# Optimization experiments

Hardware: AMD Instinct MI355X
Metric: run time of the kernel (lower is better)

## Reference

```python
import jax, jax.numpy as jnp
import numpy as np

K0, K1 = 5, 5          # patch_size
PAD = K0 // 2          # 2


def _patches(x, k0, k1):
    """x: [B, Hp, Wp, C] -> [B, Ho, Wo, C, k0*k1] sliding patches (row-major within patch)."""
    B, Hp, Wp, C = x.shape
    Ho, Wo = Hp - k0 + 1, Wp - k1 + 1
    ps = [x[:, i:i + Ho, j:j + Wo, :] for i in range(k0) for j in range(k1)]
    return jnp.stack(ps, axis=-1)


def _normalize(p):
    # per-patch zero-mean / unit (population) std over the k0*k1 patch elements
    m = jnp.mean(p, axis=-1, keepdims=True)
    s = jnp.sqrt(jnp.mean((p - m) ** 2, axis=-1, keepdims=True))
    return (p - m) / s


def setup_inputs() -> dict:
    key = jax.random.key(0)
    k1, k2 = jax.random.split(key)
    B, H, W, C = 8, 32, 32, 64
    input_1 = jax.random.normal(k1, (B, H, W, C), dtype=jnp.float32)
    input_2 = jax.random.normal(k2, (B, H, W, C), dtype=jnp.float32)
    return {"input_1": input_1, "input_2": input_2}


def reference(input_1, input_2):
    B, H, W, C = input_1.shape
    # pad input_1 by PAD on all spatial sides; input_2 by 2*PAD on rows, PAD on cols
    x1 = jnp.pad(input_1, ((0, 0), (PAD, PAD), (PAD, PAD), (0, 0)))
    x2 = jnp.pad(input_2, ((0, 0), (2 * PAD, 2 * PAD), (PAD, PAD), (0, 0)))

    P1 = _normalize(_patches(x1, K0, K1))      # [B, H, W, C, 25]
    P2 = _patches(x2, K0, K1)                  # [B, H+4, W, C, 25] (start rows 0..H+3)

    # Faithful row ordering of the original loops over input_2 patches:
    #   [0..PAD-1] ++ [PAD..H+PAD-1] ++ [H..H+PAD-1]  (rows H,H+1 duplicated; H+2,H+3 unused)
    rows_idx = np.concatenate([np.arange(PAD), np.arange(PAD, H + PAD), np.arange(H, H + PAD)])
    P2 = _normalize(P2[:, rows_idx])           # [B, H+2*PAD, W, C, 25]

    # sliding window of K0 list-rows for each output row r -> rows r..r+K0-1
    P2win = jnp.stack([P2[:, e:e + H] for e in range(K0)], axis=2)  # [B, H, K0, W, C, 25]

    # out[b,r,w,k,e,f] = sum_p P1[b,r,w,k,p] * P2win[b,r,e,f,k,p]
    out = jnp.einsum('brwkp,brefkp->brwkef', P1, P2win)  # [B, H, W, C, K0, W]
    out = out.reshape(B, H, W, C * K0 * W)
    return out  # activation is None (linear)
```

## Files before the change

### kernel.cpp

```cpp
#include <hip/hip_runtime.h>


namespace {

constexpr int OUTC = 64 * 5 * 32;

__global__ __launch_bounds__(256)
void ncc_kernel(const float* __restrict__ in1, const float* __restrict__ in2,
                float* __restrict__ out) {
    const int bid = blockIdx.x;
    const int cpair = bid & 31;
    const int r = (bid >> 5) & 31;
    const int b = bid >> 10;
    const int c0 = cpair * 2;

    __shared__ __align__(16) float x1s[2][5][36];
    __shared__ __align__(16) float x2s[2][9][36];
    __shared__ float m1s[2][32], i1s[2][32];
    __shared__ float m2s[2][5][32], i2s[2][5][32];

    const int tid = threadIdx.x;

    for (int idx = tid; idx < 2 * 5 * 36; idx += 256) {
        const int c2 = idx / 180;
        const int rem = idx - c2 * 180;
        const int i = rem / 36;
        const int pc = rem - i * 36;
        const int ir = r + i - 2;
        const int ic = pc - 2;
        float v = 0.f;
        if (ir >= 0 && ir < 32 && ic >= 0 && ic < 32)
            v = in1[((b * 32 + ir) * 32 + ic) * 64 + c0 + c2];
        x1s[c2][i][pc] = v;
    }
    for (int idx = tid; idx < 2 * 9 * 36; idx += 256) {
        const int c2 = idx / 324;
        const int rem = idx - c2 * 324;
        const int k = rem / 36;
        const int pc = rem - k * 36;
        const int ir = r + k - 4;
        const int ic = pc - 2;
        float v = 0.f;
        if (ir >= 0 && ir < 32 && ic >= 0 && ic < 32)
            v = in2[((b * 32 + ir) * 32 + ic) * 64 + c0 + c2];
        x2s[c2][k][pc] = v;
    }
    __syncthreads();

    if (tid < 64) {
        const int c2 = tid >> 5, w = tid & 31;
        float s = 0.f, ss = 0.f;
        #pragma unroll
        for (int i = 0; i < 5; ++i)
            #pragma unroll
            for (int j = 0; j < 5; ++j) {
                const float v = x1s[c2][i][w + j];
                s += v; ss += v * v;
            }
        const float m = s * (1.0f / 25.0f);
        const float var = ss * (1.0f / 25.0f) - m * m;
        m1s[c2][w] = m;
        i1s[c2][w] = 1.0f / sqrtf(fmaxf(var, 1e-30f));
    }
    for (int t = tid; t < 320; t += 256) {
        const int c2 = t / 160;
        const int rem = t - c2 * 160;
        const int e = rem >> 5;
        const int f = rem & 31;
        const int bb = (r + e <= 33) ? e : e - 2;
        float s = 0.f, ss = 0.f;
        #pragma unroll
        for (int i = 0; i < 5; ++i)
            #pragma unroll
            for (int j = 0; j < 5; ++j) {
                const float v = x2s[c2][bb + i][f + j];
                s += v; ss += v * v;
            }
        const float m = s * (1.0f / 25.0f);
        const float var = ss * (1.0f / 25.0f) - m * m;
        m2s[c2][e][f] = m;
        i2s[c2][e][f] = 1.0f / sqrtf(fmaxf(var, 1e-30f));
    }
    __syncthreads();

    const int lane = tid & 63;
    const int wave = tid >> 6;
    const int c2 = lane >> 5;
    const int f = lane & 31;
    const int wbase = wave * 8;

    int base_e[5];
    #pragma unroll
    for (int e = 0; e < 5; ++e) base_e[e] = (r + e <= 33) ? e : e - 2;

    float acc[8][5];
    #pragma unroll
    for (int wi = 0; wi < 8; ++wi)
        #pragma unroll
        for (int e = 0; e < 5; ++e) acc[wi][e] = 0.f;

    #pragma unroll
    for (int i = 0; i < 5; ++i) {
        float A[12];
        const float4* ap = reinterpret_cast<const float4*>(&x1s[c2][i][wbase]);
        const float4 a0 = ap[0], a1 = ap[1], a2 = ap[2];
        A[0] = a0.x; A[1] = a0.y; A[2]  = a0.z; A[3]  = a0.w;
        A[4] = a1.x; A[5] = a1.y; A[6]  = a1.z; A[7]  = a1.w;
        A[8] = a2.x; A[9] = a2.y; A[10] = a2.z; A[11] = a2.w;

        float Br[5][5];
        #pragma unroll
        for (int e = 0; e < 5; ++e) {
            const float* bp = &x2s[c2][base_e[e] + i][f];
            #pragma unroll
            for (int j = 0; j < 5; ++j) Br[e][j] = bp[j];
        }

        #pragma unroll
        for (int j = 0; j < 5; ++j)
            #pragma unroll
            for (int e = 0; e < 5; ++e)
                #pragma unroll
                for (int wi = 0; wi < 8; ++wi)
                    acc[wi][e] += A[wi + j] * Br[e][j];
    }

    float m2v[5], i2v[5];
    #pragma unroll
    for (int e = 0; e < 5; ++e) { m2v[e] = m2s[c2][e][f]; i2v[e] = i2s[c2][e][f]; }

    const int outrow = (b * 32 + r) * 32;
    float* op0 = out + (size_t)outrow * OUTC + (c0 + c2) * 160 + f;
    #pragma unroll
    for (int wi = 0; wi < 8; ++wi) {
        const int w = wbase + wi;
        const float m1 = m1s[c2][w];
        const float i1 = i1s[c2][w];
        float* op = op0 + (size_t)w * OUTC;
        #pragma unroll
        for (int e = 0; e < 5; ++e) {
            op[e * 32] = (acc[wi][e] - 25.0f * m1 * m2v[e]) * (i1 * i2v[e]);
        }
    }
}

}

extern "C" void kernel_launch(void* const* d_in, const int* in_sizes, int n_in,
                              void* d_out, int out_size, void* d_ws, size_t ws_size,
                              hipStream_t stream) {
    const float* in1 = (const float*)d_in[0];
    const float* in2 = (const float*)d_in[1];
    float* out = (float*)d_out;
    hipLaunchKernelGGL(ncc_kernel, dim3(8192), dim3(256), 0, stream, in1, in2, out);
}
```

Measured before the change: 373.4 us.

## Process eight channels per block with register-resident window and templated row offsets

Each block now covers 8 channels instead of 2, loading inputs with float4 vector loads. Each thread keeps the full 9x5 window of input_2 in registers and loops over all 32 output columns in groups of 4. Row-offset selection becomes compile-time template variants. This is meant to cut redundant staging and index overhead, at the cost of fewer blocks and more work and registers per thread.

```diff
diff --git a/kernel.cpp b/kernel.cpp
--- a/kernel.cpp
+++ b/kernel.cpp
@@ -5,66 +5,119 @@
 
 constexpr int OUTC = 64 * 5 * 32;
 
+template<int B0, int B1, int B2, int B3, int B4>
+__device__ __forceinline__ void compute_and_store(
+    const float (&win9)[9][5], const float* x1row,
+    const float* m1p, const float* i1p,
+    const float (&m2v)[5], const float (&i2v)[5],
+    float* opf)
+{
+    #pragma unroll 1
+    for (int wg = 0; wg < 8; ++wg) {
+        const int wbase = wg * 4;
+        float acc[4][5];
+        #pragma unroll
+        for (int wi = 0; wi < 4; ++wi)
+            #pragma unroll
+            for (int e = 0; e < 5; ++e) acc[wi][e] = 0.f;
+
+        #pragma unroll
+        for (int i = 0; i < 5; ++i) {
+            const float4 a0 = *reinterpret_cast<const float4*>(&x1row[i * 36 + wbase]);
+            const float4 a1 = *reinterpret_cast<const float4*>(&x1row[i * 36 + wbase + 4]);
+            const float A[8] = {a0.x, a0.y, a0.z, a0.w, a1.x, a1.y, a1.z, a1.w};
+            #pragma unroll
+            for (int j = 0; j < 5; ++j) {
+                #pragma unroll
+                for (int wi = 0; wi < 4; ++wi) {
+                    const float a = A[wi + j];
+                    acc[wi][0] += a * win9[B0 + i][j];
+                    acc[wi][1] += a * win9[B1 + i][j];
+                    acc[wi][2] += a * win9[B2 + i][j];
+                    acc[wi][3] += a * win9[B3 + i][j];
+                    acc[wi][4] += a * win9[B4 + i][j];
+                }
+            }
+        }
+        #pragma unroll
+        for (int wi = 0; wi < 4; ++wi) {
+            const int w = wbase + wi;
+            const float m1 = m1p[w];
+            const float i1 = i1p[w];
+            float* op = opf + (size_t)w * OUTC;
+            #pragma unroll
+            for (int e = 0; e < 5; ++e)
+                op[e * 32] = (acc[wi][e] - 25.0f * m1 * m2v[e]) * (i1 * i2v[e]);
+        }
+    }
+}
+
 __global__ __launch_bounds__(256)
 void ncc_kernel(const float* __restrict__ in1, const float* __restrict__ in2,
                 float* __restrict__ out) {
     const int bid = blockIdx.x;
-    const int cpair = bid & 31;
-    const int r = (bid >> 5) & 31;
-    const int b = bid >> 10;
-    const int c0 = cpair * 2;
+    const int c8 = bid & 7;
+    const int r  = (bid >> 3) & 31;
+    const int b  = bid >> 8;
+    const int c0 = c8 * 8;
 
-    __shared__ __align__(16) float x1s[2][5][36];
-    __shared__ __align__(16) float x2s[2][9][36];
-    __shared__ float m1s[2][32], i1s[2][32];
-    __shared__ float m2s[2][5][32], i2s[2][5][32];
+    __shared__ __align__(16) float x1s[8][5][36];
+    __shared__ __align__(16) float x2s[8][9][36];
+    __shared__ float m1s[8][32], i1s[8][32];
+    __shared__ float m2s[8][5][32], i2s[8][5][32];
 
     const int tid = threadIdx.x;
 
-    for (int idx = tid; idx < 2 * 5 * 36; idx += 256) {
-        const int c2 = idx / 180;
-        const int rem = idx - c2 * 180;
+    for (int t = tid; t < 360; t += 256) {
+        const int cg = t / 180;
+        const int rem = t - cg * 180;
         const int i = rem / 36;
         const int pc = rem - i * 36;
         const int ir = r + i - 2;
         const int ic = pc - 2;
-        float v = 0.f;
+        float4 v = make_float4(0.f, 0.f, 0.f, 0.f);
         if (ir >= 0 && ir < 32 && ic >= 0 && ic < 32)
-            v = in1[((b * 32 + ir) * 32 + ic) * 64 + c0 + c2];
-        x1s[c2][i][pc] = v;
+            v = *reinterpret_cast<const float4*>(&in1[((b * 32 + ir) * 32 + ic) * 64 + c0 + cg * 4]);
+        x1s[cg * 4 + 0][i][pc] = v.x;
+        x1s[cg * 4 + 1][i][pc] = v.y;
+        x1s[cg * 4 + 2][i][pc] = v.z;
+        x1s[cg * 4 + 3][i][pc] = v.w;
     }
-    for (int idx = tid; idx < 2 * 9 * 36; idx += 256) {
-        const int c2 = idx / 324;
-        const int rem = idx - c2 * 324;
+    for (int t = tid; t < 648; t += 256) {
+        const int cg = t / 324;
+        const int rem = t - cg * 324;
         const int k = rem / 36;
         const int pc = rem - k * 36;
         const int ir = r + k - 4;
         const int ic = pc - 2;
-        float v = 0.f;
+        float4 v = make_float4(0.f, 0.f, 0.f, 0.f);
         if (ir >= 0 && ir < 32 && ic >= 0 && ic < 32)
-            v = in2[((b * 32 + ir) * 32 + ic) * 64 + c0 + c2];
-        x2s[c2][k][pc] = v;
+            v = *reinterpret_cast<const float4*>(&in2[((b * 32 + ir) * 32 + ic) * 64 + c0 + cg * 4]);
+        x2s[cg * 4 + 0][k][pc] = v.x;
+        x2s[cg * 4 + 1][k][pc] = v.y;
+        x2s[cg * 4 + 2][k][pc] = v.z;
+        x2s[cg * 4 + 3][k][pc] = v.w;
     }
     __syncthreads();
 
-    if (tid < 64) {
-        const int c2 = tid >> 5, w = tid & 31;
+    {
+        const int ch = tid >> 5, w = tid & 31;
         float s = 0.f, ss = 0.f;
         #pragma unroll
         for (int i = 0; i < 5; ++i)
             #pragma unroll
             for (int j = 0; j < 5; ++j) {
-                const float v = x1s[c2][i][w + j];
+                const float v = x1s[ch][i][w + j];
                 s += v; ss += v * v;
             }
         const float m = s * (1.0f / 25.0f);
         const float var = ss * (1.0f / 25.0f) - m * m;
-        m1s[c2][w] = m;
-        i1s[c2][w] = 1.0f / sqrtf(fmaxf(var, 1e-30f));
+        m1s[ch][w] = m;
+        i1s[ch][w] = 1.0f / sqrtf(fmaxf(var, 1e-30f));
     }
-    for (int t = tid; t < 320; t += 256) {
-        const int c2 = t / 160;
-        const int rem = t - c2 * 160;
+    for (int t = tid; t < 1280; t += 256) {
+        const int ch = t / 160;
+        const int rem = t - ch * 160;
         const int e = rem >> 5;
         const int f = rem & 31;
         const int bb = (r + e <= 33) ? e : e - 2;
@@ -73,13 +126,13 @@
         for (int i = 0; i < 5; ++i)
             #pragma unroll
             for (int j = 0; j < 5; ++j) {
-                const float v = x2s[c2][bb + i][f + j];
+                const float v = x2s[ch][bb + i][f + j];
                 s += v; ss += v * v;
             }
         const float m = s * (1.0f / 25.0f);
         const float var = ss * (1.0f / 25.0f) - m * m;
-        m2s[c2][e][f] = m;
-        i2s[c2][e][f] = 1.0f / sqrtf(fmaxf(var, 1e-30f));
+        m2s[ch][e][f] = m;
+        i2s[ch][e][f] = 1.0f / sqrtf(fmaxf(var, 1e-30f));
     }
     __syncthreads();
 
@@ -87,61 +140,27 @@
     const int wave = tid >> 6;
     const int c2 = lane >> 5;
     const int f = lane & 31;
-    const int wbase = wave * 8;
+    const int ch = wave * 2 + c2;
 
-    int base_e[5];
+    float win9[9][5];
     #pragma unroll
-    for (int e = 0; e < 5; ++e) base_e[e] = (r + e <= 33) ? e : e - 2;
-
-    float acc[8][5];
-    #pragma unroll
-    for (int wi = 0; wi < 8; ++wi)
+    for (int k = 0; k < 9; ++k) {
+        const float* bp = &x2s[ch][k][f];
         #pragma unroll
-        for (int e = 0; e < 5; ++e) acc[wi][e] = 0.f;
-
-    #pragma unroll
-    for (int i = 0; i < 5; ++i) {
-        float A[12];
-        const float4* ap = reinterpret_cast<const float4*>(&x1s[c2][i][wbase]);
-        const float4 a0 = ap[0], a1 = ap[1], a2 = ap[2];
-        A[0] = a0.x; A[1] = a0.y; A[2]  = a0.z; A[3]  = a0.w;
-        A[4] = a1.x; A[5] = a1.y; A[6]  = a1.z; A[7]  = a1.w;
-        A[8] = a2.x; A[9] = a2.y; A[10] = a2.z; A[11] = a2.w;
-
-        float Br[5][5];
-        #pragma unroll
-        for (int e = 0; e < 5; ++e) {
-            const float* bp = &x2s[c2][base_e[e] + i][f];
-            #pragma unroll
-            for (int j = 0; j < 5; ++j) Br[e][j] = bp[j];
-        }
-
-        #pragma unroll
-        for (int j = 0; j < 5; ++j)
-            #pragma unroll
-            for (int e = 0; e < 5; ++e)
-                #pragma unroll
-                for (int wi = 0; wi < 8; ++wi)
-                    acc[wi][e] += A[wi + j] * Br[e][j];
+        for (int j = 0; j < 5; ++j) win9[k][j] = bp[j];
     }
-
     float m2v[5], i2v[5];
     #pragma unroll
-    for (int e = 0; e < 5; ++e) { m2v[e] = m2s[c2][e][f]; i2v[e] = i2s[c2][e][f]; }
+    for (int e = 0; e < 5; ++e) { m2v[e] = m2s[ch][e][f]; i2v[e] = i2s[ch][e][f]; }
 
-    const int outrow = (b * 32 + r) * 32;
-    float* op0 = out + (size_t)outrow * OUTC + (c0 + c2) * 160 + f;
-    #pragma unroll
-    for (int wi = 0; wi < 8; ++wi) {
-        const int w = wbase + wi;
-        const float m1 = m1s[c2][w];
-        const float i1 = i1s[c2][w];
-        float* op = op0 + (size_t)w * OUTC;
-        #pragma unroll
-        for (int e = 0; e < 5; ++e) {
-            op[e * 32] = (acc[wi][e] - 25.0f * m1 * m2v[e]) * (i1 * i2v[e]);
-        }
-    }
+    float* opf = out + (size_t)((b * 32 + r) * 32) * OUTC + (c0 + ch) * 160 + f;
+    const float* x1row = &x1s[ch][0][0];
+    const float* m1p = m1s[ch];
+    const float* i1p = i1s[ch];
+
+    if (r < 30)        compute_and_store<0, 1, 2, 3, 4>(win9, x1row, m1p, i1p, m2v, i2v, opf);
+    else if (r == 30)  compute_and_store<0, 1, 2, 3, 2>(win9, x1row, m1p, i1p, m2v, i2v, opf);
+    else               compute_and_store<0, 1, 2, 1, 2>(win9, x1row, m1p, i1p, m2v, i2v, opf);
 }
 
 }
@@ -152,5 +171,5 @@
     const float* in1 = (const float*)d_in[0];
     const float* in2 = (const float*)d_in[1];
     float* out = (float*)d_out;
-    hipLaunchKernelGGL(ncc_kernel, dim3(8192), dim3(256), 0, stream, in1, in2, out);
+    hipLaunchKernelGGL(ncc_kernel, dim3(2048), dim3(256), 0, stream, in1, in2, out);
 }
```

Result: faster. 355.4 us (-4.8%).
